# Kernel optimization log

Measured on AMD Instinct MI355X. Metric: run time of the kernel, lower is better.

Reference implementation:

```python
import jax, jax.numpy as jnp
import numpy as np

NEG_INF = -1e9
HIDDEN = 1024
HEADS = 16
SPH = HIDDEN // HEADS  # 64
B, Q, M = 8, 512, 512
R = Q + M


def rel_shift(x):
    # x: [N, H, Q, R] -> TransformerXL relative shift
    N, H, Qd, Rd = x.shape
    x = jnp.pad(x, ((0, 0), (0, 0), (0, 0), (1, 0)))
    x = x.reshape(N, H, Rd + 1, Qd)
    return x[:, :, 1:, :].reshape(N, H, Qd, Rd)


def setup_inputs() -> dict:
    key = jax.random.key(0)
    ks = jax.random.split(key, 11)
    std = 1.0 / np.sqrt(HIDDEN)
    # causal token mask: query position i (global pos M+i) may attend to ref pos j <= M+i
    q_pos = jnp.arange(Q)[:, None] + M
    r_pos = jnp.arange(R)[None, :]
    token_mask = (r_pos > q_pos).astype(jnp.float32)[None, None]  # [1,1,Q,R]
    return {
        "query_seqs": jax.random.normal(ks[0], (B, Q, HIDDEN), jnp.float32),
        "memory_seqs": jax.random.normal(ks[1], (B, M, HIDDEN), jnp.float32),
        "positional_encoding": jax.random.normal(ks[2], (R, HIDDEN), jnp.float32),
        "token_mask": token_mask,
        "content_bias": jax.random.normal(ks[3], (HEADS, SPH), jnp.float32) * 0.02,
        "position_bias": jax.random.normal(ks[4], (HEADS, SPH), jnp.float32) * 0.02,
        "Wq": jax.random.normal(ks[5], (HIDDEN, HEADS, SPH), jnp.float32) * std,
        "Wkc": jax.random.normal(ks[6], (HIDDEN, HEADS, SPH), jnp.float32) * std,
        "Wkp": jax.random.normal(ks[7], (HIDDEN, HEADS, SPH), jnp.float32) * std,
        "Wv": jax.random.normal(ks[8], (HIDDEN, HEADS, SPH), jnp.float32) * std,
        "Wo": jax.random.normal(ks[9], (HEADS, SPH, HIDDEN), jnp.float32) * std,
    }


def reference(query_seqs, memory_seqs, positional_encoding, token_mask,
              content_bias, position_bias, Wq, Wkc, Wkp, Wv, Wo):
    reference_seqs = jnp.concatenate([memory_seqs, query_seqs], axis=1)  # [B,R,D]
    query = jnp.einsum('nqd,dhs->nqhs', query_seqs, Wq)            # [B,Q,H,S]
    key_content = jnp.einsum('nrd,dhs->nrhs', reference_seqs, Wkc)  # [B,R,H,S]
    key_position = jnp.einsum('rd,dhs->rhs', positional_encoding, Wkp)  # [R,H,S]
    value = jnp.einsum('nrd,dhs->nrhs', reference_seqs, Wv)         # [B,R,H,S]

    content = jnp.einsum('nqhs,nrhs->nhqr', query + content_bias, key_content)
    positions = jnp.einsum('nqhs,rhs->nhqr', query + position_bias, key_position)
    positions = rel_shift(positions)

    scores = (content + positions) / np.sqrt(SPH) + token_mask * NEG_INF
    attn = jax.nn.softmax(scores, axis=3)  # [B,H,Q,R]
    out = jnp.einsum('nhqr,nrhs->nqhs', attn, value)
    return jnp.einsum('nqhs,hsd->nqd', out, Wo)  # [B,Q,D]
```

## Files before the change

### kernel.cpp

```cpp
#include <hip/hip_runtime.h>

#define B_ 8
#define Q_ 512
#define M_ 512
#define R_ 1024
#define H_ 16
#define S_ 64
#define D_ 1024
#define MEG 1048576L

typedef unsigned short ushort_t;
typedef __attribute__((ext_vector_type(8))) _Float16 f16x8;
typedef __attribute__((ext_vector_type(8))) unsigned short u16x8;
typedef __attribute__((ext_vector_type(4))) unsigned short u16x4;
typedef __attribute__((ext_vector_type(4))) float f32x4;
typedef __attribute__((ext_vector_type(2))) unsigned int u32x2;

__device__ __forceinline__ unsigned short h2u(_Float16 h) {
    union { _Float16 h; unsigned short u; } v; v.h = h; return v.u;
}
__device__ __forceinline__ unsigned int pk_f16(float a, float b) {
    union { _Float16 h[2]; unsigned int u; } v;
    v.h[0] = (_Float16)a; v.h[1] = (_Float16)b; return v.u;
}
__device__ __forceinline__ void async_cp16(const ushort_t* g, ushort_t* l) {
    __builtin_amdgcn_global_load_lds(
        (const __attribute__((address_space(1))) void*)g,
        (__attribute__((address_space(3))) void*)l, 16, 0, 0);
}

__global__ __launch_bounds__(256) void zero_out_f32_k(float* __restrict__ p, int n) {
    int i = blockIdx.x * 256 + threadIdx.x;
    if (i < n) p[i] = 0.f;
}

__global__ __launch_bounds__(256) void prep_k(
    const float* __restrict__ mem, const float* __restrict__ qry,
    const float* __restrict__ pos, const float* __restrict__ cb,
    const float* __restrict__ pb,
    const float* __restrict__ Wkc, const float* __restrict__ Wv,
    const float* __restrict__ Wkp, const float* __restrict__ Wq,
    const float* __restrict__ Wo,
    ushort_t* __restrict__ qcat, ushort_t* __restrict__ posb,
    ushort_t* __restrict__ cbpb, ushort_t* __restrict__ BT4,
    ushort_t* __restrict__ WoT) {
    int x = blockIdx.x, y = blockIdx.y, t = threadIdx.x;
    if (y < 5) {
        const float* in; ushort_t* out;
        switch (y) {
            case 0: in = Wkc; out = BT4;           break;
            case 1: in = Wv;  out = BT4 + MEG;     break;
            case 2: in = Wkp; out = BT4 + 2 * MEG; break;
            case 3: in = Wq;  out = BT4 + 3 * MEG; break;
            default: in = Wo; out = WoT;           break;
        }
        __shared__ ushort_t tile[32][33];
        int bx = (x & 31) * 32, by = (x >> 5) * 32;
        int tx = t & 31, ty = t >> 5;
        #pragma unroll
        for (int i = 0; i < 32; i += 8)
            tile[ty + i][tx] = h2u((_Float16)in[(long)(by + ty + i) * 1024 + bx + tx]);
        __syncthreads();
        #pragma unroll
        for (int i = 0; i < 32; i += 8)
            out[(long)(bx + ty + i) * 1024 + by + tx] = tile[tx][ty + i];
    } else if (y < 13) {
        int g = y - 5, r = x;
        const float* src = (r < 512) ? (mem + ((long)g * 512 + r) * 1024)
                                     : (qry + ((long)g * 512 + (r - 512)) * 1024);
        ushort_t* dst = qcat + ((long)g * 1024 + r) * 1024;
        int i = t * 4;
        f32x4 v = *(const f32x4*)(src + i);
        u32x2 o; o[0] = pk_f16(v[0], v[1]); o[1] = pk_f16(v[2], v[3]);
        *(u32x2*)(dst + i) = o;
    } else if (y == 13) {
        int i = t * 4;
        f32x4 v = *(const f32x4*)(pos + (long)x * 1024 + i);
        u32x2 o; o[0] = pk_f16(v[0], v[1]); o[1] = pk_f16(v[2], v[3]);
        *(u32x2*)(posb + (long)x * 1024 + i) = o;
    } else {
        if (x == 0) {
            for (int i = t; i < 1024; i += 256) {
                cbpb[i]        = h2u((_Float16)cb[i]);
                cbpb[1024 + i] = h2u((_Float16)pb[i]);
            }
        }
    }
}

__device__ __forceinline__ void gemm_body(const ushort_t* Arow0,
                                          const ushort_t* BTrow0,
                                          void* Crow0, long crs, int mode) {
    __shared__ __align__(16) ushort_t Al[128 * 32];
    __shared__ __align__(16) ushort_t Bl[128 * 32];

    int t = threadIdx.x;
    int wave = t >> 6, lane = t & 63, quad = lane >> 4, l16 = lane & 15;
    int wm = (wave & 1) * 64, wn = (wave >> 1) * 64;

    f32x4 acc[4][4];
    #pragma unroll
    for (int im = 0; im < 4; ++im)
        #pragma unroll
        for (int in = 0; in < 4; ++in) acc[im][in] = (f32x4){0.f, 0.f, 0.f, 0.f};

    int grow = lane >> 2, gcol = (lane & 3) * 8;
    const ushort_t* ga0 = Arow0 + (long)(wave * 32 + grow) * 1024 + gcol;
    const ushort_t* ga1 = Arow0 + (long)(wave * 32 + 16 + grow) * 1024 + gcol;
    const ushort_t* gb0 = BTrow0 + (long)(wave * 32 + grow) * 1024 + gcol;
    const ushort_t* gb1 = BTrow0 + (long)(wave * 32 + 16 + grow) * 1024 + gcol;
    ushort_t* la0 = &Al[(wave * 2 + 0) * 512];
    ushort_t* la1 = &Al[(wave * 2 + 1) * 512];
    ushort_t* lb0 = &Bl[(wave * 2 + 0) * 512];
    ushort_t* lb1 = &Bl[(wave * 2 + 1) * 512];

    for (int k0 = 0; k0 < 1024; k0 += 32) {
        __syncthreads();
        async_cp16(ga0 + k0, la0);
        async_cp16(ga1 + k0, la1);
        async_cp16(gb0 + k0, lb0);
        async_cp16(gb1 + k0, lb1);
        __syncthreads();

        f16x8 af[4], bf[4];
        #pragma unroll
        for (int im = 0; im < 4; ++im)
            af[im] = *(const f16x8*)&Al[(wm + im * 16 + l16) * 32 + quad * 8];
        #pragma unroll
        for (int in = 0; in < 4; ++in)
            bf[in] = *(const f16x8*)&Bl[(wn + in * 16 + l16) * 32 + quad * 8];
        #pragma unroll
        for (int im = 0; im < 4; ++im)
            #pragma unroll
            for (int in = 0; in < 4; ++in)
                acc[im][in] = __builtin_amdgcn_mfma_f32_16x16x32_f16(
                    af[im], bf[in], acc[im][in], 0, 0, 0);
    }

    if (mode == 2) {
        #pragma unroll
        for (int im = 0; im < 4; ++im)
            #pragma unroll
            for (int in = 0; in < 4; ++in) {
                u16x4 pk;
                #pragma unroll
                for (int reg = 0; reg < 4; ++reg) pk[reg] = h2u((_Float16)acc[im][in][reg]);
                long addr = (long)(wn + in * 16 + l16) * 1024 + wm + im * 16 + quad * 4;
                *(u16x4*)((ushort_t*)Crow0 + addr) = pk;
            }
        return;
    }
    #pragma unroll
    for (int im = 0; im < 4; ++im)
        #pragma unroll
        for (int in = 0; in < 4; ++in)
            #pragma unroll
            for (int reg = 0; reg < 4; ++reg) {
                long addr = (long)(wm + im * 16 + quad * 4 + reg) * crs
                          + wn + in * 16 + l16;
                if (mode == 1) ((float*)Crow0)[addr] = acc[im][in][reg];
                else ((ushort_t*)Crow0)[addr] = h2u((_Float16)acc[im][in][reg]);
            }
}

__global__ __launch_bounds__(256) void gemm_mega(
    const ushort_t* __restrict__ qcat, const ushort_t* __restrict__ posb,
    const ushort_t* __restrict__ BT4,
    ushort_t* __restrict__ kcC, ushort_t* __restrict__ vT,
    ushort_t* __restrict__ qproj, ushort_t* __restrict__ kpp) {
    int z = blockIdx.z;
    int x, y;
    if (z < 8) {
        int tl = blockIdx.x * 16 + blockIdx.y;
        x = tl & 7; y = tl >> 3;
    } else {
        x = blockIdx.x; y = blockIdx.y;
    }
    if (z < 8) {
        const ushort_t* Arow0 = qcat + (long)z * MEG + (long)x * 128 * 1024;
        if (y < 8) {
            gemm_body(Arow0, BT4 + (long)y * 128 * 1024,
                      kcC + (long)z * MEG + (long)x * 128 * 1024 + y * 128, 1024, 0);
        } else {
            int n0 = (y - 8) * 128;
            gemm_body(Arow0, BT4 + (long)(1024 + n0) * 1024,
                      vT + ((long)z * 1024 + n0) * 1024 + x * 128, 0, 2);
        }
    } else if (z == 8) {
        if (y >= 8) return;
        gemm_body(posb + (long)x * 128 * 1024,
                  BT4 + (long)(2048 + y * 128) * 1024,
                  kpp + (long)x * 128 * 1024 + y * 128, 1024, 0);
    } else {
        if (x >= 4 || y >= 8) return;
        int b = z - 9;
        gemm_body(qcat + (long)b * MEG + (long)(512 + x * 128) * 1024,
                  BT4 + (long)(3072 + y * 128) * 1024,
                  qproj + (long)b * 512 * 1024 + (long)x * 128 * 1024 + y * 128, 1024, 0);
    }
}

__global__ __launch_bounds__(256) void gemm_fin(
    const ushort_t* __restrict__ A, const ushort_t* __restrict__ WoT,
    float* __restrict__ out) {
    gemm_body(A + (long)blockIdx.x * 128 * 1024,
              WoT + (long)blockIdx.y * 128 * 1024,
              out + (long)blockIdx.x * 128 * 1024 + blockIdx.y * 128, 1024, 1);
}

__global__ __launch_bounds__(512) void attn_kernel(
    const ushort_t* __restrict__ qproj,
    const ushort_t* __restrict__ kc,
    const ushort_t* __restrict__ kp,
    const ushort_t* __restrict__ vT,
    const ushort_t* __restrict__ cbpb,
    ushort_t* __restrict__ aout)
{
    int qt = (blockIdx.x + ((blockIdx.y >> 6) << 1)) & 3;
    int q0 = qt * 128;
    int bh = blockIdx.y;
    int b = bh >> 4, h = bh & 15;
    int t = threadIdx.x;
    int wave = t >> 6, lane = t & 63, quad = lane >> 4, l16 = lane & 15;

    __shared__ __align__(16) ushort_t Kc[64][72];
    __shared__ __align__(16) ushort_t Vt[64][72];
    __shared__ __align__(16) ushort_t Kp[192][72];
    __shared__ __align__(16) char Pu[8][2304];
    ushort_t* Pl = (ushort_t*)&Pu[wave][0];

    const ushort_t* qrow = qproj + ((long)(b * Q_ + q0 + wave * 16 + l16)) * 1024 + h * 64;
    f16x8 qcf[2], qpf[2];
    #pragma unroll
    for (int ks = 0; ks < 2; ++ks) {
        f16x8 qv  = *(const f16x8*)(qrow + ks * 32 + quad * 8);
        f16x8 cbv = *(const f16x8*)(cbpb + h * 64 + ks * 32 + quad * 8);
        f16x8 pbv = *(const f16x8*)(cbpb + 1024 + h * 64 + ks * 32 + quad * 8);
        qcf[ks] = qv + cbv;
        qpf[ks] = qv + pbv;
    }

    float m_s[4], l_s[4];
    f32x4 o_acc[4];
    #pragma unroll
    for (int r = 0; r < 4; ++r) {
        m_s[r] = -1e30f; l_s[r] = 0.f;
        o_acc[r] = (f32x4){0.f, 0.f, 0.f, 0.f};
    }

    int srow = t >> 3, sc0 = (t & 7) * 8;
    const ushort_t* kcb = kc + ((long)(b * R_) + srow) * 1024 + h * 64 + sc0;
    const ushort_t* vtb = vT + ((long)(b * 1024 + h * 64 + srow)) * 1024 + sc0;
    const ushort_t* kpb = kp + h * 64 + sc0;

    int ntiles = ((q0 + 639) >> 6) + 1;

    u16x8 rKc = *(const u16x8*)(kcb);
    u16x8 rVt = *(const u16x8*)(vtb);
    u16x8 rKp[3];
    {
        int jb0 = 384 - q0;
        #pragma unroll
        for (int p = 0; p < 3; ++p) {
            int j = jb0 + p * 64 + srow;
            int jc = j > 1023 ? 1023 : j;
            rKp[p] = *(const u16x8*)(kpb + (long)jc * 1024);
        }
    }

    for (int it = 0; it < ntiles; ++it) {
        int r0 = it * 64;
        int jbase = r0 - q0 + 384;
        int gb0 = jbase >> 4;
        __syncthreads();
        *(u16x8*)&Kc[srow][sc0] = rKc;
        *(u16x8*)&Vt[srow][sc0] = rVt;
        if (it == 0) {
            #pragma unroll
            for (int p = 0; p < 3; ++p) {
                int j = jbase + p * 64 + srow;
                int ph = ((j >> 4) % 12) * 16 + (j & 15);
                *(u16x8*)&Kp[ph][sc0] = rKp[p];
            }
        } else {
            int j = jbase + 128 + srow;
            int ph = ((j >> 4) % 12) * 16 + (j & 15);
            *(u16x8*)&Kp[ph][sc0] = rKp[0];
        }
        __syncthreads();
        if (it + 1 < ntiles) {
            int r1 = r0 + 64;
            rKc = *(const u16x8*)(kcb + (long)r1 * 1024);
            rVt = *(const u16x8*)(vtb + r1);
            int j = r1 - q0 + 512 + srow;
            int jc = j > 1023 ? 1023 : j;
            rKp[0] = *(const u16x8*)(kpb + (long)jc * 1024);
        }

        f32x4 sc[4];
        #pragma unroll
        for (int s = 0; s < 4; ++s) sc[s] = (f32x4){0.f, 0.f, 0.f, 0.f};
        f32x4 dd[5];
        #pragma unroll
        for (int s = 0; s < 5; ++s) dd[s] = (f32x4){0.f, 0.f, 0.f, 0.f};

        __builtin_amdgcn_s_setprio(1);
        #pragma unroll
        for (int ks = 0; ks < 2; ++ks)
            #pragma unroll
            for (int sub = 0; sub < 4; ++sub) {
                f16x8 bb = *(const f16x8*)&Kc[sub * 16 + l16][ks * 32 + quad * 8];
                sc[sub] = __builtin_amdgcn_mfma_f32_16x16x32_f16(qcf[ks], bb, sc[sub], 0, 0, 0);
            }
        #pragma unroll
        for (int ks = 0; ks < 2; ++ks)
            #pragma unroll
            for (int sub = 0; sub < 5; ++sub) {
                int pb = (gb0 + 7 - wave + sub) % 12;
                f16x8 bb = *(const f16x8*)&Kp[pb * 16 + l16][ks * 32 + quad * 8];
                dd[sub] = __builtin_amdgcn_mfma_f32_16x16x32_f16(qpf[ks], bb, dd[sub], 0, 0, 0);
            }
        __builtin_amdgcn_s_setprio(0);

        #pragma unroll
        for (int reg = 0; reg < 4; ++reg) {
            int row16 = quad * 4 + reg;
            int src = (lane & 48) + ((l16 + 15 - row16) & 15);
            float dsh[5];
            #pragma unroll
            for (int sub = 0; sub < 5; ++sub)
                dsh[sub] = __shfl(dd[sub][reg], src);
            #pragma unroll
            for (int sub = 0; sub < 4; ++sub) {
                float dval = (l16 > row16) ? dsh[sub + 1] : dsh[sub];
                float sv = (sc[sub][reg] + dval) * 0.125f;
                int rl = sub * 16 + l16;
                if (r0 + rl > q0 + wave * 16 + row16 + 512) sv = -1e30f;
                sc[sub][reg] = sv;
            }
        }

        float rm[4];
        #pragma unroll
        for (int reg = 0; reg < 4; ++reg) {
            float v = fmaxf(fmaxf(sc[0][reg], sc[1][reg]), fmaxf(sc[2][reg], sc[3][reg]));
            #pragma unroll
            for (int m = 1; m < 16; m <<= 1) v = fmaxf(v, __shfl_xor(v, m));
            rm[reg] = v;
        }
        float alpha[4];
        #pragma unroll
        for (int reg = 0; reg < 4; ++reg) {
            float mn = fmaxf(m_s[reg], rm[reg]);
            alpha[reg] = __expf(m_s[reg] - mn);
            m_s[reg] = mn;
        }
        float rs[4] = {0.f, 0.f, 0.f, 0.f};
        #pragma unroll
        for (int sub = 0; sub < 4; ++sub)
            #pragma unroll
            for (int reg = 0; reg < 4; ++reg) {
                float p = __expf(sc[sub][reg] - m_s[reg]);
                rs[reg] += p;
                Pl[(quad * 4 + reg) * 72 + sub * 16 + l16] = h2u((_Float16)p);
            }
        #pragma unroll
        for (int reg = 0; reg < 4; ++reg) {
            float v = rs[reg];
            #pragma unroll
            for (int m = 1; m < 16; m <<= 1) v += __shfl_xor(v, m);
            l_s[reg] = l_s[reg] * alpha[reg] + v;
        }
        #pragma unroll
        for (int sub = 0; sub < 4; ++sub)
            #pragma unroll
            for (int reg = 0; reg < 4; ++reg)
                o_acc[sub][reg] *= alpha[reg];

        __builtin_amdgcn_s_setprio(1);
        #pragma unroll
        for (int ks = 0; ks < 2; ++ks) {
            f16x8 a = *(const f16x8*)&Pl[l16 * 72 + ks * 32 + quad * 8];
            #pragma unroll
            for (int sub = 0; sub < 4; ++sub) {
                f16x8 bb = *(const f16x8*)&Vt[sub * 16 + l16][ks * 32 + quad * 8];
                o_acc[sub] = __builtin_amdgcn_mfma_f32_16x16x32_f16(a, bb, o_acc[sub], 0, 0, 0);
            }
        }
        __builtin_amdgcn_s_setprio(0);
    }

    #pragma unroll
    for (int reg = 0; reg < 4; ++reg) {
        float inv = 1.f / l_s[reg];
        int qg = q0 + wave * 16 + quad * 4 + reg;
        ushort_t* orow = aout + ((long)(b * Q_ + qg)) * 1024 + h * 64;
        #pragma unroll
        for (int sub = 0; sub < 4; ++sub)
            orow[sub * 16 + l16] = h2u((_Float16)(o_acc[sub][reg] * inv));
    }
}

extern "C" void kernel_launch(void* const* d_in, const int* in_sizes, int n_in,
                              void* d_out, int out_size, void* d_ws, size_t ws_size,
                              hipStream_t stream) {
    const float* query  = (const float*)d_in[0];
    const float* memory = (const float*)d_in[1];
    const float* pos    = (const float*)d_in[2];
    const float* cb  = (const float*)d_in[4];
    const float* pb  = (const float*)d_in[5];
    const float* Wq  = (const float*)d_in[6];
    const float* Wkc = (const float*)d_in[7];
    const float* Wkp = (const float*)d_in[8];
    const float* Wv  = (const float*)d_in[9];
    const float* Wo  = (const float*)d_in[10];
    float* out = (float*)d_out;
    ushort_t* ws = (ushort_t*)d_ws;

    size_t ws_elems = ws_size / 2;
    if (ws_elems < 36 * MEG) {
        zero_out_f32_k<<<(out_size + 255) / 256, 256, 0, stream>>>(out, out_size);
        return;
    }

    ushort_t* cbpb  = ws;
    ushort_t* BT4   = ws + MEG;
    ushort_t* WoT   = BT4 + 4 * MEG;
    ushort_t* kpp   = WoT + MEG;
    ushort_t* posb  = kpp + MEG;
    ushort_t* qproj = posb + MEG;
    ushort_t* kcC   = qproj + 4 * MEG;
    ushort_t* vT    = kcC + 8 * MEG;
    ushort_t* qcat  = vT + 8 * MEG;
    ushort_t* aout  = qproj;

    prep_k<<<dim3(1024, 15), 256, 0, stream>>>(
        memory, query, pos, cb, pb, Wkc, Wv, Wkp, Wq, Wo,
        qcat, posb, cbpb, BT4, WoT);
    gemm_mega<<<dim3(8, 16, 17), 256, 0, stream>>>(qcat, posb, BT4, kcC, vT, qproj, kpp);
    attn_kernel<<<dim3(4, 128), 512, 0, stream>>>(qproj, kcC, kpp, vT, cbpb, aout);
    gemm_fin<<<dim3(32, 8, 1), 256, 0, stream>>>(aout, WoT, out);
}
```

Baseline: 285.9 us.

## Double-buffer GEMM LDS tiles and flatten mega-GEMM grid to skip idle blocks

Result: faster. 267.7 us (-6.4%).

```diff
diff --git a/kernel.cpp b/kernel.cpp
--- a/kernel.cpp
+++ b/kernel.cpp
@@ -91,8 +91,8 @@
 __device__ __forceinline__ void gemm_body(const ushort_t* Arow0,
                                           const ushort_t* BTrow0,
                                           void* Crow0, long crs, int mode) {
-    __shared__ __align__(16) ushort_t Al[128 * 32];
-    __shared__ __align__(16) ushort_t Bl[128 * 32];
+    __shared__ __align__(16) ushort_t Al[2][128 * 32];
+    __shared__ __align__(16) ushort_t Bl[2][128 * 32];
 
     int t = threadIdx.x;
     int wave = t >> 6, lane = t & 63, quad = lane >> 4, l16 = lane & 15;
@@ -109,32 +109,42 @@
     const ushort_t* ga1 = Arow0 + (long)(wave * 32 + 16 + grow) * 1024 + gcol;
     const ushort_t* gb0 = BTrow0 + (long)(wave * 32 + grow) * 1024 + gcol;
     const ushort_t* gb1 = BTrow0 + (long)(wave * 32 + 16 + grow) * 1024 + gcol;
-    ushort_t* la0 = &Al[(wave * 2 + 0) * 512];
-    ushort_t* la1 = &Al[(wave * 2 + 1) * 512];
-    ushort_t* lb0 = &Bl[(wave * 2 + 0) * 512];
-    ushort_t* lb1 = &Bl[(wave * 2 + 1) * 512];
-
+    int lo0 = (wave * 2 + 0) * 512;
+    int lo1 = (wave * 2 + 1) * 512;
+
+    async_cp16(ga0, &Al[0][lo0]);
+    async_cp16(ga1, &Al[0][lo1]);
+    async_cp16(gb0, &Bl[0][lo0]);
+    async_cp16(gb1, &Bl[0][lo1]);
+    __syncthreads();
+
+    int cur = 0;
     for (int k0 = 0; k0 < 1024; k0 += 32) {
-        __syncthreads();
-        async_cp16(ga0 + k0, la0);
-        async_cp16(ga1 + k0, la1);
-        async_cp16(gb0 + k0, lb0);
-        async_cp16(gb1 + k0, lb1);
-        __syncthreads();
+        int nxt = cur ^ 1;
+        if (k0 + 32 < 1024) {
+            async_cp16(ga0 + k0 + 32, &Al[nxt][lo0]);
+            async_cp16(ga1 + k0 + 32, &Al[nxt][lo1]);
+            async_cp16(gb0 + k0 + 32, &Bl[nxt][lo0]);
+            async_cp16(gb1 + k0 + 32, &Bl[nxt][lo1]);
+        }
 
         f16x8 af[4], bf[4];
         #pragma unroll
         for (int im = 0; im < 4; ++im)
-            af[im] = *(const f16x8*)&Al[(wm + im * 16 + l16) * 32 + quad * 8];
+            af[im] = *(const f16x8*)&Al[cur][(wm + im * 16 + l16) * 32 + quad * 8];
         #pragma unroll
         for (int in = 0; in < 4; ++in)
-            bf[in] = *(const f16x8*)&Bl[(wn + in * 16 + l16) * 32 + quad * 8];
+            bf[in] = *(const f16x8*)&Bl[cur][(wn + in * 16 + l16) * 32 + quad * 8];
+        __builtin_amdgcn_s_setprio(1);
         #pragma unroll
         for (int im = 0; im < 4; ++im)
             #pragma unroll
             for (int in = 0; in < 4; ++in)
                 acc[im][in] = __builtin_amdgcn_mfma_f32_16x16x32_f16(
                     af[im], bf[in], acc[im][in], 0, 0, 0);
+        __builtin_amdgcn_s_setprio(0);
+        __syncthreads();
+        cur = nxt;
     }
 
     if (mode == 2) {
@@ -168,15 +178,10 @@
     const ushort_t* __restrict__ BT4,
     ushort_t* __restrict__ kcC, ushort_t* __restrict__ vT,
     ushort_t* __restrict__ qproj, ushort_t* __restrict__ kpp) {
-    int z = blockIdx.z;
-    int x, y;
-    if (z < 8) {
-        int tl = blockIdx.x * 16 + blockIdx.y;
-        x = tl & 7; y = tl >> 3;
-    } else {
-        x = blockIdx.x; y = blockIdx.y;
-    }
-    if (z < 8) {
+    int id = blockIdx.x;
+    if (id < 1024) {
+        int z = id >> 7, tl = id & 127;
+        int x = tl >> 4, y = tl & 15;
         const ushort_t* Arow0 = qcat + (long)z * MEG + (long)x * 128 * 1024;
         if (y < 8) {
             gemm_body(Arow0, BT4 + (long)y * 128 * 1024,
@@ -186,14 +191,16 @@
             gemm_body(Arow0, BT4 + (long)(1024 + n0) * 1024,
                       vT + ((long)z * 1024 + n0) * 1024 + x * 128, 0, 2);
         }
-    } else if (z == 8) {
-        if (y >= 8) return;
+    } else if (id < 1088) {
+        int u = id - 1024;
+        int x = u >> 3, y = u & 7;
         gemm_body(posb + (long)x * 128 * 1024,
                   BT4 + (long)(2048 + y * 128) * 1024,
                   kpp + (long)x * 128 * 1024 + y * 128, 1024, 0);
     } else {
-        if (x >= 4 || y >= 8) return;
-        int b = z - 9;
+        int u = id - 1088;
+        int b = u >> 5, v2 = u & 31;
+        int x = v2 >> 3, y = v2 & 7;
         gemm_body(qcat + (long)b * MEG + (long)(512 + x * 128) * 1024,
                   BT4 + (long)(3072 + y * 128) * 1024,
                   qproj + (long)b * 512 * 1024 + (long)x * 128 * 1024 + y * 128, 1024, 0);
@@ -437,7 +444,7 @@
     prep_k<<<dim3(1024, 15), 256, 0, stream>>>(
         memory, query, pos, cb, pb, Wkc, Wv, Wkp, Wq, Wo,
         qcat, posb, cbpb, BT4, WoT);
-    gemm_mega<<<dim3(8, 16, 17), 256, 0, stream>>>(qcat, posb, BT4, kcC, vT, qproj, kpp);
+    gemm_mega<<<dim3(1344), 256, 0, stream>>>(qcat, posb, BT4, kcC, vT, qproj, kpp);
     attn_kernel<<<dim3(4, 128), 512, 0, stream>>>(qproj, kcC, kpp, vT, cbpb, aout);
     gemm_fin<<<dim3(32, 8, 1), 256, 0, stream>>>(aout, WoT, out);
 }
```
